# Kernel optimization log

Hardware: AMD Instinct MI355X
Metric: run time of the kernel (lower is better)

## Reference

```python
import jax, jax.numpy as jnp
import numpy as np

E, H, I, K, L, R, T = 8, 2048, 1024, 2, 4, 16, 4096


def setup_inputs() -> dict:
    key = jax.random.key(0)
    ks = jax.random.split(key, 10)
    s = 0.02  # realistic weight init scale
    return {
        "hidden_states": jax.random.normal(ks[0], (T, H), jnp.float32),
        "topk_weights": jax.random.uniform(ks[1], (T, K), jnp.float32),
        "w13": jax.random.normal(ks[2], (E, 2 * I, H), jnp.float32) * s,
        "w2": jax.random.normal(ks[3], (E, H, I), jnp.float32) * s,
        "gu_lora_a": jax.random.normal(ks[4], (L, E, R, H), jnp.float32) * s,
        "gu_lora_b": jax.random.normal(ks[5], (L, E, 2 * I, R), jnp.float32) * s,
        "down_lora_a": jax.random.normal(ks[6], (L, E, R, I), jnp.float32) * s,
        "down_lora_b": jax.random.normal(ks[7], (L, E, H, R), jnp.float32) * s,
        "topk_ids": jax.random.randint(ks[8], (T, K), 0, E, jnp.int32),
        "token_lora_idx": jax.random.randint(ks[9], (T,), 0, L, jnp.int32),
    }


def reference(hidden_states, topk_weights, w13, w2, gu_lora_a, gu_lora_b,
              down_lora_a, down_lora_b, topk_ids, token_lora_idx):
    # hidden_states: [T, H]; w13: [E, 2I, H]; w2: [E, H, I]
    # LoRA: gu_a [L,E,R,H], gu_b [L,E,2I,R], d_a [L,E,R,I], d_b [L,E,H,R]
    Tn, Hn = hidden_states.shape
    En, I2, _ = w13.shape
    In = I2 // 2
    Ln = gu_lora_a.shape[0]
    dt = hidden_states.dtype
    # per-token adapter one-hot [T, L] (adapter selection, constant wrt grads)
    oh_l = jax.nn.one_hot(token_lora_idx, Ln, dtype=dt)
    out = jnp.zeros((Tn, Hn), dt)
    for e in range(En):
        # combine weight for expert e per token: sum over top-k slots routed to e
        cw = jnp.sum(jnp.where(topk_ids == e, topk_weights, jnp.zeros((), dt)), axis=1)  # [T]
        # grouped gate_up GEMM (dense-masked reference form)
        h = hidden_states @ w13[e].T  # [T, 2I]
        # fused LoRA delta #1 (post gate_up, pre activation)
        u = jnp.einsum('th,lrh->tlr', hidden_states, gu_lora_a[:, e])  # [T, L, R]
        u = u * oh_l[:, :, None]  # keep only each token's adapter
        h = h + jnp.einsum('tlr,lir->ti', u, gu_lora_b[:, e])
        # SwiGLU: silu(gate) * up
        act = jax.nn.silu(h[:, :In]) * h[:, In:]  # [T, I]
        # grouped down GEMM
        d = act @ w2[e].T  # [T, H]
        # fused LoRA delta #2 (post down, pre combine)
        v = jnp.einsum('ti,lri->tlr', act, down_lora_a[:, e]) * oh_l[:, :, None]
        d = d + jnp.einsum('tlr,lhr->th', v, down_lora_b[:, e])
        # combine: weighted sum over experts
        out = out + cw[:, None] * d
    return out
```

## Files before the change

### kernel.cpp

```cpp
#include <hip/hip_runtime.h>
#include <hip/hip_bf16.h>


#define E_   8
#define H_   2048
#define I_   1024
#define I2_  2048
#define K_   2
#define L_   4
#define R_   16
#define T_   4096
#define LR_  64
#define BM   128
#define BN   128
#define BK   32
#define MAXPAD 9216
#define KTOT1 (H_ + LR_)
#define KTOT2 (I_ + LR_)

typedef __attribute__((ext_vector_type(8))) __bf16 bf16x8;
typedef __attribute__((ext_vector_type(4))) float  f32x4;

__device__ __forceinline__ unsigned short f2bf(float f) {
  union { float f; unsigned u; } v; v.f = f;
  unsigned u = v.u;
  u += 0x7fffu + ((u >> 16) & 1u);
  return (unsigned short)(u >> 16);
}
__device__ __forceinline__ unsigned pack2(float a, float b) {
  __hip_bfloat162 h = __float22bfloat162_rn(float2{a, b});
  union { __hip_bfloat162 h; unsigned u; } v; v.h = h;
  return v.u;
}
__device__ __forceinline__ float bf2f(unsigned short s) {
  union { unsigned u; float f; } v; v.u = ((unsigned)s) << 16;
  return v.f;
}
__device__ __forceinline__ void async16(const void* g, void* l) {
  __builtin_amdgcn_global_load_lds((const __attribute__((address_space(1))) void*)g,
                                   (__attribute__((address_space(3))) void*)l, 16, 0, 0);
}

__global__ void k_count(const int* __restrict__ topk_ids, int* __restrict__ cnt) {
  int i = blockIdx.x * blockDim.x + threadIdx.x;
  if (i < T_ * K_) atomicAdd(&cnt[topk_ids[i]], 1);
}

__global__ void k_prefix(const int* __restrict__ cnt, int* __restrict__ pad_off) {
  if (threadIdx.x == 0) {
    int off = 0;
    for (int e = 0; e < E_; ++e) {
      pad_off[e] = off;
      off += ((cnt[e] + BM - 1) / BM) * BM;
    }
    pad_off[E_] = off;
  }
}

__global__ void k_scatter(const int* __restrict__ topk_ids, const float* __restrict__ topk_w,
                          const int* __restrict__ tli, const int* __restrict__ pad_off,
                          int* __restrict__ cnt2, int* __restrict__ tok,
                          float* __restrict__ wgt, int* __restrict__ lidx) {
  int i = blockIdx.x * blockDim.x + threadIdx.x;
  if (i < T_ * K_) {
    int e = topk_ids[i];
    int pos = atomicAdd(&cnt2[e], 1);
    int g = pad_off[e] + pos;
    int t = i / K_;
    tok[g] = t;
    wgt[g] = topk_w[i];
    lidx[g] = tli[t];
  }
}

__global__ void k_cvt13(const float* __restrict__ w13, const float* __restrict__ gub,
                        unsigned short* __restrict__ w13x) {
  const int gr = blockIdx.x;
  const int e = gr >> 11, n = gr & (I2_ - 1);
  const int tid = threadIdx.x;
  const float* src = w13 + (size_t)gr * H_;
  unsigned short* dst = w13x + (size_t)gr * KTOT1;
#pragma unroll
  for (int c = tid; c < H_ / 4; c += 256) {
    float4 f = *(const float4*)(src + c * 4);
    *(uint2*)(dst + c * 4) = make_uint2(pack2(f.x, f.y), pack2(f.z, f.w));
  }
  if (tid < LR_) {
    const int l = tid >> 4, r = tid & 15;
    dst[H_ + tid] = f2bf(gub[(((size_t)l * E_ + e) * I2_ + n) * R_ + r]);
  }
}

__global__ void k_cvt2(const float* __restrict__ w2, const float* __restrict__ dnb,
                       unsigned short* __restrict__ w2x) {
  const int gr = blockIdx.x;
  const int e = gr >> 11, n = gr & (H_ - 1);
  const int tid = threadIdx.x;
  const float* src = w2 + (size_t)gr * I_;
  unsigned short* dst = w2x + (size_t)gr * KTOT2;
  {
    const int c = tid;
    float4 f = *(const float4*)(src + c * 4);
    *(uint2*)(dst + c * 4) = make_uint2(pack2(f.x, f.y), pack2(f.z, f.w));
  }
  if (tid < LR_) {
    const int l = tid >> 4, r = tid & 15;
    dst[I_ + tid] = f2bf(dnb[(((size_t)l * E_ + e) * H_ + n) * R_ + r]);
  }
}

__global__ void k_gather(const float* __restrict__ hidden, const int* __restrict__ tok,
                         const int* __restrict__ pad_off, const int* __restrict__ cnt,
                         unsigned short* __restrict__ x_rt) {
  const int g = blockIdx.x;
  const int tid = threadIdx.x;
  int e = -1;
#pragma unroll
  for (int i = 0; i < E_; ++i)
    if (g >= pad_off[i] && g < pad_off[i + 1]) e = i;
  const bool valid = (e >= 0) && ((g - pad_off[e]) < cnt[e]);
  const int t = valid ? tok[g] : 0;
  const float* src = hidden + (size_t)t * H_;
  unsigned short* dst = x_rt + (size_t)g * KTOT1;
#pragma unroll
  for (int c = tid; c < H_ / 4; c += 256) {
    uint2 v = make_uint2(0u, 0u);
    if (valid) {
      float4 f = *(const float4*)(src + c * 4);
      v = make_uint2(pack2(f.x, f.y), pack2(f.z, f.w));
    }
    *(uint2*)(dst + c * 4) = v;
  }
}

__global__ void k_lora_u(const float* __restrict__ hidden, const float* __restrict__ gua,
                         const int* __restrict__ tok, const int* __restrict__ lidx,
                         const int* __restrict__ pad_off, const int* __restrict__ cnt,
                         unsigned short* __restrict__ x_rt) {
  const int lane = threadIdx.x & 63;
  const int wid  = threadIdx.x >> 6;
  const int g = blockIdx.x * 4 + wid;
  int e = -1;
#pragma unroll
  for (int i = 0; i < E_; ++i)
    if (g >= pad_off[i] && g < pad_off[i + 1]) e = i;
  const bool valid = (e >= 0) && ((g - pad_off[e]) < cnt[e]);
  float sum[R_];
#pragma unroll
  for (int r = 0; r < R_; ++r) sum[r] = 0.f;
  int l = 0;
  if (valid) {
    const int t = tok[g];
    l = lidx[g];
    const float* hp = hidden + (size_t)t * H_;
    const float* ap = gua + ((size_t)l * E_ + e) * R_ * H_;
#pragma unroll
    for (int it = 0; it < H_ / 256; ++it) {
      const int k = (lane + it * 64) * 4;
      const float4 hv = *(const float4*)(hp + k);
#pragma unroll
      for (int r = 0; r < R_; ++r) {
        const float4 av = *(const float4*)(ap + (size_t)r * H_ + k);
        sum[r] += hv.x * av.x + hv.y * av.y + hv.z * av.z + hv.w * av.w;
      }
    }
#pragma unroll
    for (int r = 0; r < R_; ++r)
#pragma unroll
      for (int off = 32; off > 0; off >>= 1) sum[r] += __shfl_xor(sum[r], off);
  }
  float val = 0.f;
  if (valid && ((lane >> 4) == l)) {
    const int sr = lane & 15;
#pragma unroll
    for (int r = 0; r < R_; ++r) if (sr == r) val = sum[r];
  }
  x_rt[(size_t)g * KTOT1 + H_ + lane] = f2bf(val);
}

__global__ void k_lora_v(unsigned short* __restrict__ act, const float* __restrict__ dna,
                         const int* __restrict__ lidx, const int* __restrict__ pad_off,
                         const int* __restrict__ cnt) {
  const int lane = threadIdx.x & 63;
  const int wid  = threadIdx.x >> 6;
  const int g = blockIdx.x * 4 + wid;
  int e = -1;
#pragma unroll
  for (int i = 0; i < E_; ++i)
    if (g >= pad_off[i] && g < pad_off[i + 1]) e = i;
  const bool valid = (e >= 0) && ((g - pad_off[e]) < cnt[e]);
  float sum[R_];
#pragma unroll
  for (int r = 0; r < R_; ++r) sum[r] = 0.f;
  int l = 0;
  if (valid) {
    l = lidx[g];
    const unsigned short* av_p = act + (size_t)g * KTOT2;
    const float* ap = dna + ((size_t)l * E_ + e) * R_ * I_;
#pragma unroll
    for (int it = 0; it < I_ / 256; ++it) {
      const int k = (lane + it * 64) * 4;
      const ushort4 a4 = *(const ushort4*)(av_p + k);
      const float ax = bf2f(a4.x), ay = bf2f(a4.y), az = bf2f(a4.z), aw = bf2f(a4.w);
#pragma unroll
      for (int r = 0; r < R_; ++r) {
        const float4 av = *(const float4*)(ap + (size_t)r * I_ + k);
        sum[r] += ax * av.x + ay * av.y + az * av.z + aw * av.w;
      }
    }
#pragma unroll
    for (int r = 0; r < R_; ++r)
#pragma unroll
      for (int off = 32; off > 0; off >>= 1) sum[r] += __shfl_xor(sum[r], off);
  }
  float val = 0.f;
  if (valid && ((lane >> 4) == l)) {
    const int sr = lane & 15;
#pragma unroll
    for (int r = 0; r < R_; ++r) if (sr == r) val = sum[r];
  }
  act[(size_t)g * KTOT2 + I_ + lane] = f2bf(val);
}

__global__ __launch_bounds__(256, 2)
void k_gemm1(const unsigned short* __restrict__ x_rt, const unsigned short* __restrict__ w13x,
             const int* __restrict__ pad_off, unsigned short* __restrict__ act) {
  __shared__ __align__(16) unsigned short sA [BM * BK];
  __shared__ __align__(16) unsigned short sBg[BN * BK];
  __shared__ __align__(16) unsigned short sBu[BN * BK];

  const int base = blockIdx.y * BM;
  if (base >= pad_off[E_]) return;
  int e = 0;
#pragma unroll
  for (int i = 1; i < E_; ++i) if (base >= pad_off[i]) e = i;
  const int n0 = blockIdx.x * BN;

  const int tid  = threadIdx.x;
  const int lane = tid & 63;
  const int wid  = tid >> 6;
  const int wm   = (wid >> 1) * 64;
  const int wn   = (wid & 1) * 64;
  const int quad = lane >> 4;
  const int mr   = lane & 15;

  const int srow = tid >> 2, spc = (tid & 3) * 8;
  const unsigned short* aS0  = x_rt + (size_t)(base + srow) * KTOT1 + spc;
  const unsigned short* aS1  = aS0 + (size_t)64 * KTOT1;
  const unsigned short* bgS0 = w13x + ((size_t)e * I2_ + n0 + srow) * KTOT1 + spc;
  const unsigned short* bgS1 = bgS0 + (size_t)64 * KTOT1;
  const unsigned short* buS0 = bgS0 + (size_t)I_ * KTOT1;
  const unsigned short* buS1 = buS0 + (size_t)64 * KTOT1;
  unsigned short* aD  = sA  + wid * 512;
  unsigned short* bgD = sBg + wid * 512;
  unsigned short* buD = sBu + wid * 512;

  f32x4 zero = {0.f, 0.f, 0.f, 0.f};
  f32x4 accg[4][4], accu[4][4];
#pragma unroll
  for (int i = 0; i < 4; ++i)
#pragma unroll
    for (int j = 0; j < 4; ++j) { accg[i][j] = zero; accu[i][j] = zero; }

  for (int kt = 0; kt < KTOT1; kt += BK) {
    async16(aS0,  aD);        async16(aS1,  aD + 2048);
    async16(bgS0, bgD);       async16(bgS1, bgD + 2048);
    async16(buS0, buD);       async16(buS1, buD + 2048);
    aS0 += BK; aS1 += BK; bgS0 += BK; bgS1 += BK; buS0 += BK; buS1 += BK;
    __syncthreads();

    bf16x8 af[4], bg[4], bu[4];
#pragma unroll
    for (int i = 0; i < 4; ++i)
      af[i] = *(const bf16x8*)&sA[(wm + i * 16 + mr) * BK + quad * 8];
#pragma unroll
    for (int j = 0; j < 4; ++j) {
      bg[j] = *(const bf16x8*)&sBg[(wn + j * 16 + mr) * BK + quad * 8];
      bu[j] = *(const bf16x8*)&sBu[(wn + j * 16 + mr) * BK + quad * 8];
    }
#pragma unroll
    for (int i = 0; i < 4; ++i)
#pragma unroll
      for (int j = 0; j < 4; ++j) {
        accg[i][j] = __builtin_amdgcn_mfma_f32_16x16x32_bf16(af[i], bg[j], accg[i][j], 0, 0, 0);
        accu[i][j] = __builtin_amdgcn_mfma_f32_16x16x32_bf16(af[i], bu[j], accu[i][j], 0, 0, 0);
      }
    __syncthreads();
  }

#pragma unroll
  for (int i = 0; i < 4; ++i)
#pragma unroll
    for (int j = 0; j < 4; ++j)
#pragma unroll
      for (int r = 0; r < 4; ++r) {
        const int m = wm + i * 16 + quad * 4 + r;
        const int n = wn + j * 16 + mr;
        const float gv = accg[i][j][r];
        const float uv = accu[i][j][r];
        const float s = gv / (1.f + __expf(-gv));
        act[(size_t)(base + m) * KTOT2 + (n0 + n)] = f2bf(s * uv);
      }
}

__global__ __launch_bounds__(256, 2)
void k_gemm2(const unsigned short* __restrict__ act, const unsigned short* __restrict__ w2x,
             const int* __restrict__ tok, const float* __restrict__ wgt,
             const int* __restrict__ pad_off, const int* __restrict__ cnt,
             float* __restrict__ out) {
  __shared__ __align__(16) unsigned short sA[BM * BK];
  __shared__ __align__(16) unsigned short sB[BN * BK];

  const int base = blockIdx.y * BM;
  if (base >= pad_off[E_]) return;
  int e = 0;
#pragma unroll
  for (int i = 1; i < E_; ++i) if (base >= pad_off[i]) e = i;
  const int erow0 = pad_off[e];
  const int cnt_e = cnt[e];
  const int n0 = blockIdx.x * BN;

  const int tid  = threadIdx.x;
  const int lane = tid & 63;
  const int wid  = tid >> 6;
  const int wm   = (wid >> 1) * 64;
  const int wn   = (wid & 1) * 64;
  const int quad = lane >> 4;
  const int mr   = lane & 15;

  const int srow = tid >> 2, spc = (tid & 3) * 8;
  const unsigned short* aS0 = act + (size_t)(base + srow) * KTOT2 + spc;
  const unsigned short* aS1 = aS0 + (size_t)64 * KTOT2;
  const unsigned short* bS0 = w2x + ((size_t)e * H_ + n0 + srow) * KTOT2 + spc;
  const unsigned short* bS1 = bS0 + (size_t)64 * KTOT2;
  unsigned short* aD = sA + wid * 512;
  unsigned short* bD = sB + wid * 512;

  f32x4 zero = {0.f, 0.f, 0.f, 0.f};
  f32x4 acc[4][4];
#pragma unroll
  for (int i = 0; i < 4; ++i)
#pragma unroll
    for (int j = 0; j < 4; ++j) acc[i][j] = zero;

  for (int kt = 0; kt < KTOT2; kt += BK) {
    async16(aS0, aD);  async16(aS1, aD + 2048);
    async16(bS0, bD);  async16(bS1, bD + 2048);
    aS0 += BK; aS1 += BK; bS0 += BK; bS1 += BK;
    __syncthreads();

    bf16x8 af[4], bb[4];
#pragma unroll
    for (int i = 0; i < 4; ++i)
      af[i] = *(const bf16x8*)&sA[(wm + i * 16 + mr) * BK + quad * 8];
#pragma unroll
    for (int j = 0; j < 4; ++j)
      bb[j] = *(const bf16x8*)&sB[(wn + j * 16 + mr) * BK + quad * 8];
#pragma unroll
    for (int i = 0; i < 4; ++i)
#pragma unroll
      for (int j = 0; j < 4; ++j)
        acc[i][j] = __builtin_amdgcn_mfma_f32_16x16x32_bf16(af[i], bb[j], acc[i][j], 0, 0, 0);
    __syncthreads();
  }

#pragma unroll
  for (int i = 0; i < 4; ++i)
#pragma unroll
    for (int j = 0; j < 4; ++j)
#pragma unroll
      for (int r = 0; r < 4; ++r) {
        const int m = wm + i * 16 + quad * 4 + r;
        const int g = base + m;
        if ((g - erow0) < cnt_e) {
          const int n = wn + j * 16 + mr;
          atomicAdd(&out[(size_t)tok[g] * H_ + (n0 + n)], wgt[g] * acc[i][j][r]);
        }
      }
}

extern "C" void kernel_launch(void* const* d_in, const int* in_sizes, int n_in,
                              void* d_out, int out_size, void* d_ws, size_t ws_size,
                              hipStream_t stream) {
  const float* hidden  = (const float*)d_in[0];
  const float* topk_w  = (const float*)d_in[1];
  const float* w13     = (const float*)d_in[2];
  const float* w2      = (const float*)d_in[3];
  const float* gua     = (const float*)d_in[4];
  const float* gub     = (const float*)d_in[5];
  const float* dna     = (const float*)d_in[6];
  const float* dnb     = (const float*)d_in[7];
  const int*   topk_id = (const int*)d_in[8];
  const int*   tli     = (const int*)d_in[9];
  float* out = (float*)d_out;

  char* ws = (char*)d_ws;
  int*   cnt     = (int*)(ws + 0);
  int*   cnt2    = (int*)(ws + 32);
  int*   pad_off = (int*)(ws + 64);
  size_t off = 256;
  int*   tok  = (int*)(ws + off);   off += 4 * MAXPAD;
  float* wgt  = (float*)(ws + off); off += 4 * MAXPAD;
  int*   lidx = (int*)(ws + off);   off += 4 * MAXPAD;
  unsigned short* x_rt = (unsigned short*)(ws + off); off += (size_t)2 * MAXPAD * KTOT1;
  unsigned short* act  = (unsigned short*)(ws + off); off += (size_t)2 * MAXPAD * KTOT2;
  unsigned short* w13x = (unsigned short*)(ws + off); off += (size_t)2 * E_ * I2_ * KTOT1;
  unsigned short* w2x  = (unsigned short*)(ws + off); off += (size_t)2 * E_ * H_ * KTOT2;

  hipMemsetAsync(d_ws, 0, 256, stream);
  hipMemsetAsync(d_out, 0, (size_t)T_ * H_ * sizeof(float), stream);

  k_count  <<<dim3((T_ * K_ + 255) / 256), dim3(256), 0, stream>>>(topk_id, cnt);
  k_prefix <<<dim3(1), dim3(64), 0, stream>>>(cnt, pad_off);
  k_scatter<<<dim3((T_ * K_ + 255) / 256), dim3(256), 0, stream>>>(topk_id, topk_w, tli, pad_off,
                                                                   cnt2, tok, wgt, lidx);
  k_cvt13  <<<dim3(E_ * I2_), dim3(256), 0, stream>>>(w13, gub, w13x);
  k_cvt2   <<<dim3(E_ * H_), dim3(256), 0, stream>>>(w2, dnb, w2x);
  k_gather <<<dim3(MAXPAD), dim3(256), 0, stream>>>(hidden, tok, pad_off, cnt, x_rt);
  k_lora_u <<<dim3(MAXPAD / 4), dim3(256), 0, stream>>>(hidden, gua, tok, lidx, pad_off, cnt, x_rt);
  k_gemm1  <<<dim3(I_ / BN, MAXPAD / BM), dim3(256), 0, stream>>>(x_rt, w13x, pad_off, act);
  k_lora_v <<<dim3(MAXPAD / 4), dim3(256), 0, stream>>>(act, dna, lidx, pad_off, cnt);
  k_gemm2  <<<dim3(H_ / BN, MAXPAD / BM), dim3(256), 0, stream>>>(act, w2x, tok, wgt,
                                                                  pad_off, cnt, out);
}
```

Before: 808.3 us.

## Compute LoRA shrink projections with MFMA tile GEMM over all adapters

Replaces the per-token scalar wave-reduction LoRA-A kernels with a templated bf16 MFMA GEMM. Each 128-row tile of routed tokens is multiplied against all four adapters' A matrices for its expert, and the non-selected adapters are masked to zero at store time. The LoRA-A weights are pre-converted to bf16 in a per-expert layout inside the existing conversion kernels. This computes four times the LoRA FLOPs and reads A in bf16 instead of fp32 activations, in exchange for matrix-core throughput and far fewer redundant fp32 weight loads. Launch bounds on the main GEMMs are also raised to 4 waves per SIMD.

Result: slower. 1.396 ms (+72.7%).

```diff
diff --git a/kernel.cpp b/kernel.cpp
--- a/kernel.cpp
+++ b/kernel.cpp
@@ -32,10 +32,6 @@
   union { __hip_bfloat162 h; unsigned u; } v; v.h = h;
   return v.u;
 }
-__device__ __forceinline__ float bf2f(unsigned short s) {
-  union { unsigned u; float f; } v; v.u = ((unsigned)s) << 16;
-  return v.f;
-}
 __device__ __forceinline__ void async16(const void* g, void* l) {
   __builtin_amdgcn_global_load_lds((const __attribute__((address_space(1))) void*)g,
                                    (__attribute__((address_space(3))) void*)l, 16, 0, 0);
@@ -73,39 +69,65 @@
   }
 }
 
-__global__ void k_cvt13(const float* __restrict__ w13, const float* __restrict__ gub,
-                        unsigned short* __restrict__ w13x) {
-  const int gr = blockIdx.x;
-  const int e = gr >> 11, n = gr & (I2_ - 1);
+__global__ void k_cvtA(const float* __restrict__ w13, const float* __restrict__ gub,
+                       const float* __restrict__ gua,
+                       unsigned short* __restrict__ w13x, unsigned short* __restrict__ gua_x) {
+  const int bid = blockIdx.x;
   const int tid = threadIdx.x;
-  const float* src = w13 + (size_t)gr * H_;
-  unsigned short* dst = w13x + (size_t)gr * KTOT1;
-#pragma unroll
-  for (int c = tid; c < H_ / 4; c += 256) {
-    float4 f = *(const float4*)(src + c * 4);
-    *(uint2*)(dst + c * 4) = make_uint2(pack2(f.x, f.y), pack2(f.z, f.w));
-  }
-  if (tid < LR_) {
-    const int l = tid >> 4, r = tid & 15;
-    dst[H_ + tid] = f2bf(gub[(((size_t)l * E_ + e) * I2_ + n) * R_ + r]);
-  }
-}
-
-__global__ void k_cvt2(const float* __restrict__ w2, const float* __restrict__ dnb,
-                       unsigned short* __restrict__ w2x) {
-  const int gr = blockIdx.x;
-  const int e = gr >> 11, n = gr & (H_ - 1);
+  if (bid < E_ * I2_) {
+    const int e = bid >> 11, n = bid & (I2_ - 1);
+    const float* src = w13 + (size_t)bid * H_;
+    unsigned short* dst = w13x + (size_t)bid * KTOT1;
+#pragma unroll
+    for (int c = tid; c < H_ / 4; c += 256) {
+      float4 f = *(const float4*)(src + c * 4);
+      *(uint2*)(dst + c * 4) = make_uint2(pack2(f.x, f.y), pack2(f.z, f.w));
+    }
+    if (tid < LR_) {
+      const int l = tid >> 4, r = tid & 15;
+      dst[H_ + tid] = f2bf(gub[(((size_t)l * E_ + e) * I2_ + n) * R_ + r]);
+    }
+  } else {
+    const int idx = bid - E_ * I2_;
+    const int e = idx >> 6, n = idx & 63;
+    const int l = n >> 4, r = n & 15;
+    const float* src = gua + (((size_t)l * E_ + e) * R_ + r) * H_;
+    unsigned short* dst = gua_x + ((size_t)e * LR_ + n) * H_;
+#pragma unroll
+    for (int c = tid; c < H_ / 4; c += 256) {
+      float4 f = *(const float4*)(src + c * 4);
+      *(uint2*)(dst + c * 4) = make_uint2(pack2(f.x, f.y), pack2(f.z, f.w));
+    }
+  }
+}
+
+__global__ void k_cvtB(const float* __restrict__ w2, const float* __restrict__ dnb,
+                       const float* __restrict__ dna,
+                       unsigned short* __restrict__ w2x, unsigned short* __restrict__ dna_x) {
+  const int bid = blockIdx.x;
   const int tid = threadIdx.x;
-  const float* src = w2 + (size_t)gr * I_;
-  unsigned short* dst = w2x + (size_t)gr * KTOT2;
-  {
-    const int c = tid;
-    float4 f = *(const float4*)(src + c * 4);
-    *(uint2*)(dst + c * 4) = make_uint2(pack2(f.x, f.y), pack2(f.z, f.w));
-  }
-  if (tid < LR_) {
-    const int l = tid >> 4, r = tid & 15;
-    dst[I_ + tid] = f2bf(dnb[(((size_t)l * E_ + e) * H_ + n) * R_ + r]);
+  if (bid < E_ * H_) {
+    const int e = bid >> 11, n = bid & (H_ - 1);
+    const float* src = w2 + (size_t)bid * I_;
+    unsigned short* dst = w2x + (size_t)bid * KTOT2;
+    {
+      float4 f = *(const float4*)(src + tid * 4);
+      *(uint2*)(dst + tid * 4) = make_uint2(pack2(f.x, f.y), pack2(f.z, f.w));
+    }
+    if (tid < LR_) {
+      const int l = tid >> 4, r = tid & 15;
+      dst[I_ + tid] = f2bf(dnb[(((size_t)l * E_ + e) * H_ + n) * R_ + r]);
+    }
+  } else {
+    const int idx = bid - E_ * H_;
+    const int e = idx >> 6, n = idx & 63;
+    const int l = n >> 4, r = n & 15;
+    const float* src = dna + (((size_t)l * E_ + e) * R_ + r) * I_;
+    unsigned short* dst = dna_x + ((size_t)e * LR_ + n) * I_;
+    {
+      float4 f = *(const float4*)(src + tid * 4);
+      *(uint2*)(dst + tid * 4) = make_uint2(pack2(f.x, f.y), pack2(f.z, f.w));
+    }
   }
 }
 
@@ -133,96 +155,78 @@
   }
 }
 
-__global__ void k_lora_u(const float* __restrict__ hidden, const float* __restrict__ gua,
-                         const int* __restrict__ tok, const int* __restrict__ lidx,
-                         const int* __restrict__ pad_off, const int* __restrict__ cnt,
-                         unsigned short* __restrict__ x_rt) {
-  const int lane = threadIdx.x & 63;
-  const int wid  = threadIdx.x >> 6;
-  const int g = blockIdx.x * 4 + wid;
-  int e = -1;
-#pragma unroll
-  for (int i = 0; i < E_; ++i)
-    if (g >= pad_off[i] && g < pad_off[i + 1]) e = i;
-  const bool valid = (e >= 0) && ((g - pad_off[e]) < cnt[e]);
-  float sum[R_];
-#pragma unroll
-  for (int r = 0; r < R_; ++r) sum[r] = 0.f;
-  int l = 0;
-  if (valid) {
-    const int t = tok[g];
-    l = lidx[g];
-    const float* hp = hidden + (size_t)t * H_;
-    const float* ap = gua + ((size_t)l * E_ + e) * R_ * H_;
-#pragma unroll
-    for (int it = 0; it < H_ / 256; ++it) {
-      const int k = (lane + it * 64) * 4;
-      const float4 hv = *(const float4*)(hp + k);
-#pragma unroll
-      for (int r = 0; r < R_; ++r) {
-        const float4 av = *(const float4*)(ap + (size_t)r * H_ + k);
-        sum[r] += hv.x * av.x + hv.y * av.y + hv.z * av.z + hv.w * av.w;
+template <int KDIM, int RSTRIDE, int KOFS>
+__global__ __launch_bounds__(256, 4)
+void k_lora_gemm(const unsigned short* __restrict__ X, const unsigned short* __restrict__ A,
+                 const int* __restrict__ lidx, const int* __restrict__ pad_off,
+                 const int* __restrict__ cnt, unsigned short* __restrict__ dst) {
+  __shared__ __align__(16) unsigned short sA[BM * BK];
+  __shared__ __align__(16) unsigned short sB[LR_ * BK];
+
+  const int base = blockIdx.x * BM;
+  if (base >= pad_off[E_]) return;
+  int e = 0;
+#pragma unroll
+  for (int i = 1; i < E_; ++i) if (base >= pad_off[i]) e = i;
+  const int erow0 = pad_off[e];
+  const int cnt_e = cnt[e];
+
+  const int tid  = threadIdx.x;
+  const int lane = tid & 63;
+  const int wid  = tid >> 6;
+  const int wm   = wid * 32;
+  const int quad = lane >> 4;
+  const int mr   = lane & 15;
+
+  const unsigned short* aS0 = X + (size_t)(base + (tid >> 2)) * RSTRIDE + (tid & 3) * 8;
+  const unsigned short* aS1 = aS0 + (size_t)64 * RSTRIDE;
+  const unsigned short* bS  = A + ((size_t)e * LR_ + (tid >> 2)) * KDIM + (tid & 3) * 8;
+  unsigned short* aD = sA + wid * 512;
+  unsigned short* bD = sB + wid * 512;
+
+  f32x4 zero = {0.f, 0.f, 0.f, 0.f};
+  f32x4 acc[2][4];
+#pragma unroll
+  for (int i = 0; i < 2; ++i)
+#pragma unroll
+    for (int j = 0; j < 4; ++j) acc[i][j] = zero;
+
+  for (int kt = 0; kt < KDIM; kt += BK) {
+    async16(aS0, aD);  async16(aS1, aD + 2048);
+    async16(bS,  bD);
+    aS0 += BK; aS1 += BK; bS += BK;
+    __syncthreads();
+
+    bf16x8 af[2], bb[4];
+#pragma unroll
+    for (int i = 0; i < 2; ++i)
+      af[i] = *(const bf16x8*)&sA[(wm + i * 16 + mr) * BK + quad * 8];
+#pragma unroll
+    for (int j = 0; j < 4; ++j)
+      bb[j] = *(const bf16x8*)&sB[(j * 16 + mr) * BK + quad * 8];
+#pragma unroll
+    for (int i = 0; i < 2; ++i)
+#pragma unroll
+      for (int j = 0; j < 4; ++j)
+        acc[i][j] = __builtin_amdgcn_mfma_f32_16x16x32_bf16(af[i], bb[j], acc[i][j], 0, 0, 0);
+    __syncthreads();
+  }
+
+#pragma unroll
+  for (int i = 0; i < 2; ++i)
+#pragma unroll
+    for (int j = 0; j < 4; ++j)
+#pragma unroll
+      for (int r = 0; r < 4; ++r) {
+        const int m = wm + i * 16 + quad * 4 + r;
+        const int g = base + m;
+        const bool valid = ((g - erow0) < cnt_e) && (lidx[g] == j);
+        const float v = valid ? acc[i][j][r] : 0.f;
+        dst[(size_t)g * RSTRIDE + KOFS + j * 16 + mr] = f2bf(v);
       }
-    }
-#pragma unroll
-    for (int r = 0; r < R_; ++r)
-#pragma unroll
-      for (int off = 32; off > 0; off >>= 1) sum[r] += __shfl_xor(sum[r], off);
-  }
-  float val = 0.f;
-  if (valid && ((lane >> 4) == l)) {
-    const int sr = lane & 15;
-#pragma unroll
-    for (int r = 0; r < R_; ++r) if (sr == r) val = sum[r];
-  }
-  x_rt[(size_t)g * KTOT1 + H_ + lane] = f2bf(val);
-}
-
-__global__ void k_lora_v(unsigned short* __restrict__ act, const float* __restrict__ dna,
-                         const int* __restrict__ lidx, const int* __restrict__ pad_off,
-                         const int* __restrict__ cnt) {
-  const int lane = threadIdx.x & 63;
-  const int wid  = threadIdx.x >> 6;
-  const int g = blockIdx.x * 4 + wid;
-  int e = -1;
-#pragma unroll
-  for (int i = 0; i < E_; ++i)
-    if (g >= pad_off[i] && g < pad_off[i + 1]) e = i;
-  const bool valid = (e >= 0) && ((g - pad_off[e]) < cnt[e]);
-  float sum[R_];
-#pragma unroll
-  for (int r = 0; r < R_; ++r) sum[r] = 0.f;
-  int l = 0;
-  if (valid) {
-    l = lidx[g];
-    const unsigned short* av_p = act + (size_t)g * KTOT2;
-    const float* ap = dna + ((size_t)l * E_ + e) * R_ * I_;
-#pragma unroll
-    for (int it = 0; it < I_ / 256; ++it) {
-      const int k = (lane + it * 64) * 4;
-      const ushort4 a4 = *(const ushort4*)(av_p + k);
-      const float ax = bf2f(a4.x), ay = bf2f(a4.y), az = bf2f(a4.z), aw = bf2f(a4.w);
-#pragma unroll
-      for (int r = 0; r < R_; ++r) {
-        const float4 av = *(const float4*)(ap + (size_t)r * I_ + k);
-        sum[r] += ax * av.x + ay * av.y + az * av.z + aw * av.w;
-      }
-    }
-#pragma unroll
-    for (int r = 0; r < R_; ++r)
-#pragma unroll
-      for (int off = 32; off > 0; off >>= 1) sum[r] += __shfl_xor(sum[r], off);
-  }
-  float val = 0.f;
-  if (valid && ((lane >> 4) == l)) {
-    const int sr = lane & 15;
-#pragma unroll
-    for (int r = 0; r < R_; ++r) if (sr == r) val = sum[r];
-  }
-  act[(size_t)g * KTOT2 + I_ + lane] = f2bf(val);
-}
-
-__global__ __launch_bounds__(256, 2)
+}
+
+__global__ __launch_bounds__(256, 4)
 void k_gemm1(const unsigned short* __restrict__ x_rt, const unsigned short* __restrict__ w13x,
              const int* __restrict__ pad_off, unsigned short* __restrict__ act) {
   __shared__ __align__(16) unsigned short sA [BM * BK];
@@ -303,7 +307,7 @@
       }
 }
 
-__global__ __launch_bounds__(256, 2)
+__global__ __launch_bounds__(256, 4)
 void k_gemm2(const unsigned short* __restrict__ act, const unsigned short* __restrict__ w2x,
              const int* __restrict__ tok, const float* __restrict__ wgt,
              const int* __restrict__ pad_off, const int* __restrict__ cnt,
@@ -402,10 +406,12 @@
   int*   tok  = (int*)(ws + off);   off += 4 * MAXPAD;
   float* wgt  = (float*)(ws + off); off += 4 * MAXPAD;
   int*   lidx = (int*)(ws + off);   off += 4 * MAXPAD;
-  unsigned short* x_rt = (unsigned short*)(ws + off); off += (size_t)2 * MAXPAD * KTOT1;
-  unsigned short* act  = (unsigned short*)(ws + off); off += (size_t)2 * MAXPAD * KTOT2;
-  unsigned short* w13x = (unsigned short*)(ws + off); off += (size_t)2 * E_ * I2_ * KTOT1;
-  unsigned short* w2x  = (unsigned short*)(ws + off); off += (size_t)2 * E_ * H_ * KTOT2;
+  unsigned short* x_rt  = (unsigned short*)(ws + off); off += (size_t)2 * MAXPAD * KTOT1;
+  unsigned short* act   = (unsigned short*)(ws + off); off += (size_t)2 * MAXPAD * KTOT2;
+  unsigned short* w13x  = (unsigned short*)(ws + off); off += (size_t)2 * E_ * I2_ * KTOT1;
+  unsigned short* w2x   = (unsigned short*)(ws + off); off += (size_t)2 * E_ * H_ * KTOT2;
+  unsigned short* gua_x = (unsigned short*)(ws + off); off += (size_t)2 * E_ * LR_ * H_;
+  unsigned short* dna_x = (unsigned short*)(ws + off); off += (size_t)2 * E_ * LR_ * I_;
 
   hipMemsetAsync(d_ws, 0, 256, stream);
   hipMemsetAsync(d_out, 0, (size_t)T_ * H_ * sizeof(float), stream);
@@ -414,12 +420,14 @@
   k_prefix <<<dim3(1), dim3(64), 0, stream>>>(cnt, pad_off);
   k_scatter<<<dim3((T_ * K_ + 255) / 256), dim3(256), 0, stream>>>(topk_id, topk_w, tli, pad_off,
                                                                    cnt2, tok, wgt, lidx);
-  k_cvt13  <<<dim3(E_ * I2_), dim3(256), 0, stream>>>(w13, gub, w13x);
-  k_cvt2   <<<dim3(E_ * H_), dim3(256), 0, stream>>>(w2, dnb, w2x);
+  k_cvtA   <<<dim3(E_ * I2_ + E_ * LR_), dim3(256), 0, stream>>>(w13, gub, gua, w13x, gua_x);
+  k_cvtB   <<<dim3(E_ * H_ + E_ * LR_), dim3(256), 0, stream>>>(w2, dnb, dna, w2x, dna_x);
   k_gather <<<dim3(MAXPAD), dim3(256), 0, stream>>>(hidden, tok, pad_off, cnt, x_rt);
-  k_lora_u <<<dim3(MAXPAD / 4), dim3(256), 0, stream>>>(hidden, gua, tok, lidx, pad_off, cnt, x_rt);
+  k_lora_gemm<H_, KTOT1, H_><<<dim3(MAXPAD / BM), dim3(256), 0, stream>>>(
+      x_rt, gua_x, lidx, pad_off, cnt, x_rt);
   k_gemm1  <<<dim3(I_ / BN, MAXPAD / BM), dim3(256), 0, stream>>>(x_rt, w13x, pad_off, act);
-  k_lora_v <<<dim3(MAXPAD / 4), dim3(256), 0, stream>>>(act, dna, lidx, pad_off, cnt);
+  k_lora_gemm<I_, KTOT2, I_><<<dim3(MAXPAD / BM), dim3(256), 0, stream>>>(
+      act, dna_x, lidx, pad_off, cnt, act);
   k_gemm2  <<<dim3(H_ / BN, MAXPAD / BM), dim3(256), 0, stream>>>(act, w2x, tok, wgt,
                                                                   pad_off, cnt, out);
 }
```
